# Kernel optimization log

Hardware: AMD Instinct MI355X
Metric: run time of the kernel (lower is better)

The kernel has to match this reference:

```python
import jax, jax.numpy as jnp
import numpy as np
from jax import lax

EPS = 1e-5


def _st_gcn_layer(x, w, b, A):
    # x: (N, C, T, V); w: (K*Co, C, 9, 1); A: (K, V, V) (already scaled by edge importance)
    y = lax.conv_general_dilated(x, w, window_strides=(1, 1),
                                 padding=[(4, 4), (0, 0)],
                                 dimension_numbers=('NCHW', 'OIHW', 'NCHW'))
    y = y + b[None, :, None, None]
    N, KC, T, V = y.shape
    K = A.shape[0]
    y = y.reshape(N, K, KC // K, T, V)
    y = jnp.einsum('nkctv,kvw->nctw', y, A)  # graph convolution
    return jax.nn.relu(y)


def setup_inputs() -> dict:
    key = jax.random.key(0)
    ks = jax.random.split(key, 8)
    N, T, V, C, Co, K, KT = 16, 512, 25, 256, 256, 3, 9
    x = jax.random.normal(ks[0], (N, T, V, C), dtype=jnp.float32)
    bn_gamma = jax.random.uniform(ks[1], (V * C,), dtype=jnp.float32)
    bn_beta = jax.random.normal(ks[2], (V * C,), dtype=jnp.float32)
    bn_mean = jnp.zeros((V * C,), dtype=jnp.float32)
    bn_var = jnp.ones((V * C,), dtype=jnp.float32)
    w_scale = 1.0 / np.sqrt(C * KT)
    w1 = jax.random.normal(ks[3], (K * Co, C, KT, 1), dtype=jnp.float32) * w_scale
    b1 = jax.random.normal(ks[4], (K * Co,), dtype=jnp.float32) * 0.01
    w2 = jax.random.normal(ks[5], (K * Co, Co, KT, 1), dtype=jnp.float32) * w_scale
    b2 = jax.random.normal(ks[6], (K * Co,), dtype=jnp.float32) * 0.01
    ei1 = jnp.ones((K, V, V), dtype=jnp.float32)
    ei2 = jnp.ones((K, V, V), dtype=jnp.float32)
    A = jax.random.uniform(ks[7], (K, V, V), dtype=jnp.float32)
    return {"x": x, "bn_gamma": bn_gamma, "bn_beta": bn_beta, "bn_mean": bn_mean,
            "bn_var": bn_var, "w1": w1, "b1": b1, "ei1": ei1, "w2": w2, "b2": b2,
            "ei2": ei2, "A": A}


def reference(x, bn_gamma, bn_beta, bn_mean, bn_var, w1, b1, ei1, w2, b2, ei2, A):
    N, T, V, C = x.shape
    # data_bn over V*C channels (V-major, C-minor per the torch permutes), eval mode
    xb = jnp.transpose(x, (0, 2, 3, 1)).reshape(N, V * C, T)  # (N, V*C, T)
    inv = bn_gamma / jnp.sqrt(bn_var + EPS)
    xb = (xb - bn_mean[None, :, None]) * inv[None, :, None] + bn_beta[None, :, None]
    xb = jnp.transpose(xb.reshape(N, V, C, T), (0, 2, 3, 1))  # (N, C, T, V)
    h = _st_gcn_layer(xb, w1, b1, A * ei1)
    h = _st_gcn_layer(h, w2, b2, A * ei2)
    return jnp.transpose(h, (0, 2, 3, 1))  # (N, T, V, Cout)
```

## Files before the change

### kernel.cpp

```cpp
#include <hip/hip_runtime.h>
#include <stdint.h>

typedef unsigned short ushortT;
typedef short short8 __attribute__((ext_vector_type(8)));
typedef float f32x4 __attribute__((ext_vector_type(4)));
typedef unsigned short us4 __attribute__((ext_vector_type(4)));

#define TP 520
#define PAD 4
#define XTILE_B (264 * 64)
#define ATILE_B (128 * 64)

__device__ __forceinline__ unsigned short f2bf(float f) {
  union { float f; unsigned int u; } v; v.f = f;
  unsigned int r = (v.u + 0x7fffu + ((v.u >> 16) & 1u)) >> 16;
  return (unsigned short)r;
}
__device__ __forceinline__ float bf2f(unsigned short b) {
  union { unsigned int u; float f; } v; v.u = ((unsigned int)b) << 16;
  return v.f;
}
__device__ __forceinline__ float ldadp(const void* p, long i, int bf) {
  return bf ? bf2f(((const unsigned short*)p)[i]) : ((const float*)p)[i];
}

__device__ __forceinline__ void gload16(const void* g, void* l) {
  __builtin_amdgcn_global_load_lds(
      (const __attribute__((address_space(1))) void*)g,
      (__attribute__((address_space(3))) void*)l, 16, 0, 0);
}

__global__ void detect_kernel(const void* var, int* flags) {
  flags[0] = (((const unsigned int*)var)[0] == 0x3F803F80u) ? 1 : 0;
}

__global__ void prep_w_kernel(const void* w, ushortT* __restrict__ Wt, const int* flags) {
  int bf = flags[0];
  long i = (long)blockIdx.x * 256 + threadIdx.x;
  int c = (int)(i & 255);
  long mc = i >> 8;
  int m = (int)(mc % 768);
  int dt = (int)(mc / 768);
  long dst = (((long)(dt * 8 + (c >> 5)) * 768 + m) << 5) + (c & 31);
  Wt[dst] = f2bf(ldadp(w, ((long)m * 256 + c) * 9 + dt, bf));
}

__global__ void prep_ae_kernel(const void* A, const void* ei, const void* b,
                               float* __restrict__ Ae, float* __restrict__ Bsum,
                               const int* flags) {
  __shared__ float ash[1875];
  int bf = flags[0];
  int tid = threadIdx.x;
  for (int i = tid; i < 1875; i += 1024) {
    float ae = ldadp(A, i, bf) * ldadp(ei, i, bf);
    ash[i] = ae; Ae[i] = ae;
  }
  __syncthreads();
  for (int i = tid; i < 6400; i += 1024) {
    int c = i / 25, w = i % 25;
    float s = 0.f;
    for (int k = 0; k < 3; k++) {
      float cs = 0.f;
      for (int v = 0; v < 25; v++) cs += ash[(k * 25 + v) * 25 + w];
      s += ldadp(b, k * 256 + c, bf) * cs;
    }
    Bsum[i] = s;
  }
}

__global__ void pad_kernel(ushortT* __restrict__ Xb) {
  long nv = (long)blockIdx.y * 25 + blockIdx.x;
  int tid = threadIdx.x;
  #pragma unroll
  for (int r = 0; r < 4; r++) {
    Xb[(nv * TP + r) * 256 + tid] = 0;
    Xb[(nv * TP + 516 + r) * 256 + tid] = 0;
  }
}

__global__ void bn_kernel(const void* x, long xoff, const void* gamma, const void* beta,
                          const void* mean, const void* var, const int* flags,
                          ushortT* __restrict__ Xb, long total) {
  long i = (long)blockIdx.x * 256 + threadIdx.x;
  if (i >= total) return;
  int bf = flags[0];
  int c = (int)(i & 255);
  long j = i >> 8;
  int v = (int)(j % 25); j /= 25;
  int t = (int)(j % 512); j /= 512;
  int nl = (int)j;
  int pc = v * 256 + c;
  float inv = ldadp(gamma, pc, bf) * rsqrtf(ldadp(var, pc, bf) + 1e-5f);
  float val = (ldadp(x, xoff + i, bf) - ldadp(mean, pc, bf)) * inv + ldadp(beta, pc, bf);
  Xb[(((long)(nl * 25 + v)) * TP + t + PAD) * 256 + c] = f2bf(val);
}

__global__ __launch_bounds__(256, 2) void conv_kernel(
    const ushortT* __restrict__ Xb, const ushortT* __restrict__ Wt,
    ushortT* __restrict__ Y) {
  __shared__ short8 smem[(2 * XTILE_B + 2 * ATILE_B) / 16];
  char* lds = (char*)smem;
  char* Xl0 = lds;
  char* Xl1 = lds + XTILE_B;
  char* Al0 = lds + 2 * XTILE_B;
  char* Al1 = lds + 2 * XTILE_B + ATILE_B;

  const int tid = threadIdx.x;
  const int lane = tid & 63;
  const int wave = tid >> 6;
  const int wm = wave >> 1, wn = wave & 1;
  const int kb = lane >> 4;
  const int l15 = lane & 15;
  const int wubase = (tid & ~63);

  int bid = blockIdx.x;
  const int v = bid % 25;
  const int rtile = bid / 25;
  const int tt = rtile & 1;
  const int mt = rtile >> 1;
  const int nl = blockIdx.y;
  const int m0 = mt * 128;
  const int t0 = tt * 256;

  const long xrowbase = ((long)(nl * 25 + v)) * TP + t0;

  auto stageX = [&](int cc, char* xb) {
    #pragma unroll
    for (int k = 0; k < 4; k++) {
      int s = k * 256 + tid;
      int r = s >> 2, q = s & 3;
      gload16(Xb + (xrowbase + r) * 256 + cc * 32 + q * 8,
              xb + (long)(k * 256 + wubase) * 16);
    }
    if (tid < 32) {
      int s = 1024 + tid;
      int r = s >> 2, q = s & 3;
      gload16(Xb + (xrowbase + r) * 256 + cc * 32 + q * 8,
              xb + (long)1024 * 16);
    }
  };
  auto stageA = [&](int cc, int dt, char* ab) {
    const ushortT* wb = Wt + (((long)(dt * 8 + cc) * 768 + m0) << 5);
    #pragma unroll
    for (int k = 0; k < 2; k++) {
      int s = k * 256 + tid;
      gload16(wb + (long)s * 8, ab + (long)(k * 256 + wubase) * 16);
    }
  };

  f32x4 acc[4][8];
  #pragma unroll
  for (int i = 0; i < 4; i++)
    #pragma unroll
    for (int j = 0; j < 8; j++) { acc[i][j][0]=0.f; acc[i][j][1]=0.f; acc[i][j][2]=0.f; acc[i][j][3]=0.f; }

  stageX(0, Xl0);
  stageA(0, 0, Al0);
  __syncthreads();

  for (int cc = 0; cc < 8; cc++) {
    char* Xcur = (cc & 1) ? Xl1 : Xl0;
    for (int dt = 0; dt < 9; dt++) {
      const int ks = cc * 9 + dt;
      if (dt == 0 && cc < 7) stageX(cc + 1, (cc & 1) ? Xl0 : Xl1);
      if (ks < 71) {
        int nk = ks + 1;
        stageA(nk / 9, nk % 9, (nk & 1) ? Al1 : Al0);
      }

      char* Acur = (ks & 1) ? Al1 : Al0;
      short8 a[4], b[8];
      #pragma unroll
      for (int i = 0; i < 4; i++) {
        int r = wm * 64 + i * 16 + l15;
        a[i] = *(const short8*)(Acur + r * 64 + kb * 16);
      }
      #pragma unroll
      for (int j = 0; j < 8; j++) {
        int r = wn * 128 + j * 16 + l15 + dt;
        b[j] = *(const short8*)(Xcur + r * 64 + kb * 16);
      }
      #pragma unroll
      for (int i = 0; i < 4; i++)
        #pragma unroll
        for (int j = 0; j < 8; j++)
          acc[i][j] = __builtin_amdgcn_mfma_f32_16x16x32_bf16(a[i], b[j], acc[i][j], 0, 0, 0);

      __syncthreads();
    }
  }

  #pragma unroll
  for (int i = 0; i < 4; i++) {
    #pragma unroll
    for (int j = 0; j < 8; j++) {
      int tg = t0 + wn * 128 + j * 16 + l15;
      int kc = m0 + wm * 64 + i * 16 + (kb << 2);
      long off = (((long)(nl * 512 + tg)) * 25 + v) * 768 + kc;
      us4 u;
      u[0] = f2bf(acc[i][j][0]);
      u[1] = f2bf(acc[i][j][1]);
      u[2] = f2bf(acc[i][j][2]);
      u[3] = f2bf(acc[i][j][3]);
      *(us4*)(Y + off) = u;
    }
  }
}

__global__ __launch_bounds__(256) void gconv_kernel(
    const ushortT* __restrict__ Y, const float* __restrict__ Ae,
    const float* __restrict__ Bsum, ushortT* __restrict__ dstb,
    float* __restrict__ dstf, int mode) {
  __shared__ float aesh[1875];
  const int tid = threadIdx.x;
  const int nl = blockIdx.y;
  const int t0 = blockIdx.x << 2;
  for (int i = tid; i < 1875; i += 256) aesh[i] = Ae[i];
  __syncthreads();

  float acc[4][25];
  #pragma unroll
  for (int w = 0; w < 25; w++) {
    float bs = Bsum[tid * 25 + w];
    acc[0][w] = bs; acc[1][w] = bs; acc[2][w] = bs; acc[3][w] = bs;
  }
  for (int k = 0; k < 3; k++) {
    for (int v = 0; v < 25; v++) {
      long ybase = (((long)(nl * 512 + t0)) * 25 + v) * 768 + k * 256 + tid;
      float y0 = bf2f(Y[ybase]);
      float y1 = bf2f(Y[ybase + 1L * 25 * 768]);
      float y2 = bf2f(Y[ybase + 2L * 25 * 768]);
      float y3 = bf2f(Y[ybase + 3L * 25 * 768]);
      const float* ap = &aesh[(k * 25 + v) * 25];
      #pragma unroll
      for (int w = 0; w < 25; w++) {
        float a = ap[w];
        acc[0][w] = fmaf(y0, a, acc[0][w]);
        acc[1][w] = fmaf(y1, a, acc[1][w]);
        acc[2][w] = fmaf(y2, a, acc[2][w]);
        acc[3][w] = fmaf(y3, a, acc[3][w]);
      }
    }
  }
  #pragma unroll
  for (int t = 0; t < 4; t++) {
    #pragma unroll
    for (int w = 0; w < 25; w++) {
      float vv = acc[t][w];
      vv = vv > 0.f ? vv : 0.f;
      if (mode == 0) {
        long off = (((long)(nl * 25 + w)) * TP + (t0 + t) + PAD) * 256 + tid;
        dstb[off] = f2bf(vv);
      } else {
        long off = (((long)(nl * 512 + (t0 + t))) * 25 + w) * 256 + tid;
        dstf[off] = vv;
      }
    }
  }
}

extern "C" void kernel_launch(void* const* d_in, const int* in_sizes, int n_in,
                              void* d_out, int out_size, void* d_ws, size_t ws_size,
                              hipStream_t stream) {
  const void* x     = d_in[0];
  const void* gamma = d_in[1];
  const void* beta  = d_in[2];
  const void* mean  = d_in[3];
  const void* var   = d_in[4];
  const void* w1    = d_in[5];
  const void* b1    = d_in[6];
  const void* ei1   = d_in[7];
  const void* w2    = d_in[8];
  const void* b2    = d_in[9];
  const void* ei2   = d_in[10];
  const void* A     = d_in[11];
  float* out = (float*)d_out;

  const size_t WtB  = 9L * 768 * 256 * 2;
  const size_t XbB1 = 25L * TP * 256 * 2;
  const size_t YB1  = 512L * 25 * 768 * 2;
  const size_t fixed = 256 + 2 * WtB + 2 * (1875 * 4) + 2 * (6400 * 4) + 8 * 256;

  int G = 16;
  while (G > 1 && fixed + (size_t)G * (XbB1 + YB1) > ws_size) G >>= 1;

  char* ws = (char*)d_ws;
  size_t off = 0;
  auto alloc = [&](size_t bytes) { char* p = ws + off; off = (off + bytes + 255) & ~(size_t)255; return p; };
  int* flags   = (int*)alloc(256);
  ushortT* Wt1 = (ushortT*)alloc(WtB);
  ushortT* Wt2 = (ushortT*)alloc(WtB);
  float* Ae1   = (float*)alloc(1875 * 4);
  float* Ae2   = (float*)alloc(1875 * 4);
  float* Bs1   = (float*)alloc(6400 * 4);
  float* Bs2   = (float*)alloc(6400 * 4);
  ushortT* Xb  = (ushortT*)alloc((size_t)G * XbB1);
  ushortT* Y   = (ushortT*)alloc((size_t)G * YB1);

  detect_kernel<<<1, 1, 0, stream>>>(var, flags);
  prep_w_kernel<<<6912, 256, 0, stream>>>(w1, Wt1, flags);
  prep_w_kernel<<<6912, 256, 0, stream>>>(w2, Wt2, flags);
  prep_ae_kernel<<<1, 1024, 0, stream>>>(A, ei1, b1, Ae1, Bs1, flags);
  prep_ae_kernel<<<1, 1024, 0, stream>>>(A, ei2, b2, Ae2, Bs2, flags);

  for (int n0 = 0; n0 < 16; n0 += G) {
    long xoff = (long)n0 * 512 * 25 * 256;
    float* out_c = out + (size_t)n0 * 512 * 25 * 256;
    long total = (long)G * 512 * 25 * 256;

    pad_kernel<<<dim3(25, G), 256, 0, stream>>>(Xb);
    bn_kernel<<<(int)((total + 255) / 256), 256, 0, stream>>>(x, xoff, gamma, beta, mean, var, flags, Xb, total);

    conv_kernel<<<dim3(300, G), 256, 0, stream>>>(Xb, Wt1, Y);
    gconv_kernel<<<dim3(128, G), 256, 0, stream>>>(Y, Ae1, Bs1, Xb, (float*)nullptr, 0);
    conv_kernel<<<dim3(300, G), 256, 0, stream>>>(Xb, Wt2, Y);
    gconv_kernel<<<dim3(128, G), 256, 0, stream>>>(Y, Ae2, Bs2, (ushortT*)nullptr, out_c, 1);
  }
}
```

Baseline: 1.832 ms.

## Swizzle conv LDS tiles, stage weight pairs per barrier, vectorize BN and gconv

```diff
diff --git a/kernel.cpp b/kernel.cpp
--- a/kernel.cpp
+++ b/kernel.cpp
@@ -4,12 +4,14 @@
 typedef unsigned short ushortT;
 typedef short short8 __attribute__((ext_vector_type(8)));
 typedef float f32x4 __attribute__((ext_vector_type(4)));
+typedef float f32x2 __attribute__((ext_vector_type(2)));
 typedef unsigned short us4 __attribute__((ext_vector_type(4)));
 
 #define TP 520
 #define PAD 4
 #define XTILE_B (264 * 64)
 #define ATILE_B (128 * 64)
+#define APAIR_B (2 * ATILE_B)
 
 __device__ __forceinline__ unsigned short f2bf(float f) {
   union { float f; unsigned int u; } v; v.f = f;
@@ -22,6 +24,17 @@
 }
 __device__ __forceinline__ float ldadp(const void* p, long i, int bf) {
   return bf ? bf2f(((const unsigned short*)p)[i]) : ((const float*)p)[i];
+}
+__device__ __forceinline__ f32x2 ldadp2(const void* p, long i, int bf) {
+  f32x2 r;
+  if (bf) {
+    unsigned int u = *(const unsigned int*)((const unsigned short*)p + i);
+    r[0] = bf2f((unsigned short)(u & 0xffffu));
+    r[1] = bf2f((unsigned short)(u >> 16));
+  } else {
+    r = *(const f32x2*)((const float*)p + i);
+  }
+  return r;
 }
 
 __device__ __forceinline__ void gload16(const void* g, void* l) {
@@ -81,29 +94,33 @@
 __global__ void bn_kernel(const void* x, long xoff, const void* gamma, const void* beta,
                           const void* mean, const void* var, const int* flags,
                           ushortT* __restrict__ Xb, long total) {
-  long i = (long)blockIdx.x * 256 + threadIdx.x;
-  if (i >= total) return;
+  long i2 = ((long)blockIdx.x * 256 + threadIdx.x) * 2;
+  if (i2 >= total) return;
   int bf = flags[0];
-  int c = (int)(i & 255);
-  long j = i >> 8;
+  int c = (int)(i2 & 255);
+  long j = i2 >> 8;
   int v = (int)(j % 25); j /= 25;
   int t = (int)(j % 512); j /= 512;
   int nl = (int)j;
   int pc = v * 256 + c;
-  float inv = ldadp(gamma, pc, bf) * rsqrtf(ldadp(var, pc, bf) + 1e-5f);
-  float val = (ldadp(x, xoff + i, bf) - ldadp(mean, pc, bf)) * inv + ldadp(beta, pc, bf);
-  Xb[(((long)(nl * 25 + v)) * TP + t + PAD) * 256 + c] = f2bf(val);
+  f32x2 xv = ldadp2(x, xoff + i2, bf);
+  unsigned int outw = 0;
+  #pragma unroll
+  for (int e = 0; e < 2; e++) {
+    float inv = ldadp(gamma, pc + e, bf) * rsqrtf(ldadp(var, pc + e, bf) + 1e-5f);
+    float val = (xv[e] - ldadp(mean, pc + e, bf)) * inv + ldadp(beta, pc + e, bf);
+    outw |= ((unsigned int)f2bf(val)) << (16 * e);
+  }
+  *(unsigned int*)(Xb + (((long)(nl * 25 + v)) * TP + t + PAD) * 256 + c) = outw;
 }
 
 __global__ __launch_bounds__(256, 2) void conv_kernel(
     const ushortT* __restrict__ Xb, const ushortT* __restrict__ Wt,
     ushortT* __restrict__ Y) {
-  __shared__ short8 smem[(2 * XTILE_B + 2 * ATILE_B) / 16];
+  __shared__ short8 smem[(2 * XTILE_B + 2 * APAIR_B) / 16];
   char* lds = (char*)smem;
-  char* Xl0 = lds;
-  char* Xl1 = lds + XTILE_B;
-  char* Al0 = lds + 2 * XTILE_B;
-  char* Al1 = lds + 2 * XTILE_B + ATILE_B;
+  char* Xl[2] = { lds, lds + XTILE_B };
+  char* Ap[2] = { lds + 2 * XTILE_B, lds + 2 * XTILE_B + APAIR_B };
 
   const int tid = threadIdx.x;
   const int lane = tid & 63;
@@ -129,22 +146,29 @@
     for (int k = 0; k < 4; k++) {
       int s = k * 256 + tid;
       int r = s >> 2, q = s & 3;
-      gload16(Xb + (xrowbase + r) * 256 + cc * 32 + q * 8,
+      int ql = q ^ ((r >> 1) & 3);
+      gload16(Xb + (xrowbase + r) * 256 + cc * 32 + ql * 8,
               xb + (long)(k * 256 + wubase) * 16);
     }
     if (tid < 32) {
       int s = 1024 + tid;
       int r = s >> 2, q = s & 3;
-      gload16(Xb + (xrowbase + r) * 256 + cc * 32 + q * 8,
+      int ql = q ^ ((r >> 1) & 3);
+      gload16(Xb + (xrowbase + r) * 256 + cc * 32 + ql * 8,
               xb + (long)1024 * 16);
     }
   };
-  auto stageA = [&](int cc, int dt, char* ab) {
-    const ushortT* wb = Wt + (((long)(dt * 8 + cc) * 768 + m0) << 5);
-    #pragma unroll
-    for (int k = 0; k < 2; k++) {
-      int s = k * 256 + tid;
-      gload16(wb + (long)s * 8, ab + (long)(k * 256 + wubase) * 16);
+  auto stageA = [&](int cc, int dt0, int cnt, char* ab) {
+    for (int d = 0; d < cnt; d++) {
+      const ushortT* wb = Wt + (((long)((dt0 + d) * 8 + cc) * 768 + m0) << 5);
+      #pragma unroll
+      for (int k = 0; k < 2; k++) {
+        int s = k * 256 + tid;
+        int r = s >> 2, q = s & 3;
+        int ql = q ^ ((r >> 1) & 3);
+        gload16(wb + (long)(r * 4 + ql) * 8,
+                ab + (long)d * ATILE_B + (long)(k * 256 + wubase) * 16);
+      }
     }
   };
 
@@ -154,38 +178,44 @@
     #pragma unroll
     for (int j = 0; j < 8; j++) { acc[i][j][0]=0.f; acc[i][j][1]=0.f; acc[i][j][2]=0.f; acc[i][j][3]=0.f; }
 
-  stageX(0, Xl0);
-  stageA(0, 0, Al0);
+  stageX(0, Xl[0]);
+  stageA(0, 0, 2, Ap[0]);
   __syncthreads();
 
   for (int cc = 0; cc < 8; cc++) {
-    char* Xcur = (cc & 1) ? Xl1 : Xl0;
-    for (int dt = 0; dt < 9; dt++) {
-      const int ks = cc * 9 + dt;
-      if (dt == 0 && cc < 7) stageX(cc + 1, (cc & 1) ? Xl0 : Xl1);
-      if (ks < 71) {
-        int nk = ks + 1;
-        stageA(nk / 9, nk % 9, (nk & 1) ? Al1 : Al0);
-      }
-
-      char* Acur = (ks & 1) ? Al1 : Al0;
-      short8 a[4], b[8];
-      #pragma unroll
-      for (int i = 0; i < 4; i++) {
-        int r = wm * 64 + i * 16 + l15;
-        a[i] = *(const short8*)(Acur + r * 64 + kb * 16);
-      }
-      #pragma unroll
-      for (int j = 0; j < 8; j++) {
-        int r = wn * 128 + j * 16 + l15 + dt;
-        b[j] = *(const short8*)(Xcur + r * 64 + kb * 16);
-      }
-      #pragma unroll
-      for (int i = 0; i < 4; i++)
+    char* Xcur = Xl[cc & 1];
+    for (int sub = 0; sub < 5; sub++) {
+      const int p = cc * 5 + sub;
+      if (sub == 0 && cc < 7) stageX(cc + 1, Xl[(cc + 1) & 1]);
+      if (p < 39) {
+        int np = p + 1;
+        int ncc = np / 5, nsub = np % 5;
+        stageA(ncc, (nsub < 4) ? 2 * nsub : 8, (nsub < 4) ? 2 : 1, Ap[np & 1]);
+      }
+
+      const char* Acur = Ap[p & 1];
+      const int ndt = (sub < 4) ? 2 : 1;
+      for (int d = 0; d < ndt; d++) {
+        const int dt = 2 * sub + d;
+        short8 a[4], b[8];
         #pragma unroll
-        for (int j = 0; j < 8; j++)
-          acc[i][j] = __builtin_amdgcn_mfma_f32_16x16x32_bf16(a[i], b[j], acc[i][j], 0, 0, 0);
-
+        for (int i = 0; i < 4; i++) {
+          int r = wm * 64 + i * 16 + l15;
+          int sl = kb ^ ((r >> 1) & 3);
+          a[i] = *(const short8*)(Acur + d * ATILE_B + r * 64 + sl * 16);
+        }
+        #pragma unroll
+        for (int j = 0; j < 8; j++) {
+          int r = wn * 128 + j * 16 + l15 + dt;
+          int sl = kb ^ ((r >> 1) & 3);
+          b[j] = *(const short8*)(Xcur + r * 64 + sl * 16);
+        }
+        #pragma unroll
+        for (int i = 0; i < 4; i++)
+          #pragma unroll
+          for (int j = 0; j < 8; j++)
+            acc[i][j] = __builtin_amdgcn_mfma_f32_16x16x32_bf16(a[i], b[j], acc[i][j], 0, 0, 0);
+      }
       __syncthreads();
     }
   }
@@ -213,47 +243,55 @@
     float* __restrict__ dstf, int mode) {
   __shared__ float aesh[1875];
   const int tid = threadIdx.x;
+  const int cp = tid & 127;
+  const int c  = cp * 2;
+  const int th = tid >> 7;
   const int nl = blockIdx.y;
   const int t0 = blockIdx.x << 2;
+  const int tA = t0 + 2 * th;
   for (int i = tid; i < 1875; i += 256) aesh[i] = Ae[i];
   __syncthreads();
 
-  float acc[4][25];
+  float acc[2][2][25];
   #pragma unroll
   for (int w = 0; w < 25; w++) {
-    float bs = Bsum[tid * 25 + w];
-    acc[0][w] = bs; acc[1][w] = bs; acc[2][w] = bs; acc[3][w] = bs;
+    float b0 = Bsum[c * 25 + w], b1 = Bsum[(c + 1) * 25 + w];
+    acc[0][0][w] = b0; acc[0][1][w] = b0;
+    acc[1][0][w] = b1; acc[1][1][w] = b1;
   }
   for (int k = 0; k < 3; k++) {
     for (int v = 0; v < 25; v++) {
-      long ybase = (((long)(nl * 512 + t0)) * 25 + v) * 768 + k * 256 + tid;
-      float y0 = bf2f(Y[ybase]);
-      float y1 = bf2f(Y[ybase + 1L * 25 * 768]);
-      float y2 = bf2f(Y[ybase + 2L * 25 * 768]);
-      float y3 = bf2f(Y[ybase + 3L * 25 * 768]);
+      long ybase = (((long)(nl * 512 + tA)) * 25 + v) * 768 + k * 256 + c;
+      unsigned int ua = *(const unsigned int*)(Y + ybase);
+      unsigned int ub = *(const unsigned int*)(Y + ybase + 25L * 768);
+      float ya0 = bf2f((unsigned short)(ua & 0xffffu));
+      float ya1 = bf2f((unsigned short)(ua >> 16));
+      float yb0 = bf2f((unsigned short)(ub & 0xffffu));
+      float yb1 = bf2f((unsigned short)(ub >> 16));
       const float* ap = &aesh[(k * 25 + v) * 25];
       #pragma unroll
       for (int w = 0; w < 25; w++) {
         float a = ap[w];
-        acc[0][w] = fmaf(y0, a, acc[0][w]);
-        acc[1][w] = fmaf(y1, a, acc[1][w]);
-        acc[2][w] = fmaf(y2, a, acc[2][w]);
-        acc[3][w] = fmaf(y3, a, acc[3][w]);
-      }
-    }
-  }
-  #pragma unroll
-  for (int t = 0; t < 4; t++) {
+        acc[0][0][w] = fmaf(ya0, a, acc[0][0][w]);
+        acc[1][0][w] = fmaf(ya1, a, acc[1][0][w]);
+        acc[0][1][w] = fmaf(yb0, a, acc[0][1][w]);
+        acc[1][1][w] = fmaf(yb1, a, acc[1][1][w]);
+      }
+    }
+  }
+  #pragma unroll
+  for (int tt = 0; tt < 2; tt++) {
+    int t = tA + tt;
     #pragma unroll
     for (int w = 0; w < 25; w++) {
-      float vv = acc[t][w];
-      vv = vv > 0.f ? vv : 0.f;
+      float v0 = acc[0][tt][w]; v0 = v0 > 0.f ? v0 : 0.f;
+      float v1 = acc[1][tt][w]; v1 = v1 > 0.f ? v1 : 0.f;
       if (mode == 0) {
-        long off = (((long)(nl * 25 + w)) * TP + (t0 + t) + PAD) * 256 + tid;
-        dstb[off] = f2bf(vv);
+        unsigned int pk = (unsigned int)f2bf(v0) | ((unsigned int)f2bf(v1) << 16);
+        *(unsigned int*)(dstb + (((long)(nl * 25 + w)) * TP + t + PAD) * 256 + c) = pk;
       } else {
-        long off = (((long)(nl * 512 + (t0 + t))) * 25 + w) * 256 + tid;
-        dstf[off] = vv;
+        f32x2 pk; pk[0] = v0; pk[1] = v1;
+        *(f32x2*)(dstf + (((long)(nl * 512 + t)) * 25 + w) * 256 + c) = pk;
       }
     }
   }
@@ -309,7 +347,7 @@
     long total = (long)G * 512 * 25 * 256;
 
     pad_kernel<<<dim3(25, G), 256, 0, stream>>>(Xb);
-    bn_kernel<<<(int)((total + 255) / 256), 256, 0, stream>>>(x, xoff, gamma, beta, mean, var, flags, Xb, total);
+    bn_kernel<<<(int)((total / 2 + 255) / 256), 256, 0, stream>>>(x, xoff, gamma, beta, mean, var, flags, Xb, total);
 
     conv_kernel<<<dim3(300, G), 256, 0, stream>>>(Xb, Wt1, Y);
     gconv_kernel<<<dim3(128, G), 256, 0, stream>>>(Y, Ae1, Bs1, Xb, (float*)nullptr, 0);
```

New measurement: 2.021 ms. 10.3% more time.
